# Kernel optimization log

Measured on AMD Instinct MI355X. Metric: run time of the kernel, lower is better.

Reference implementation:

```python
import jax, jax.numpy as jnp
import numpy as np

N_NODES = 100000
N_EDGES = 640000
D = 128
N_LAYERS = 4
N_GRAPHS = 512


def setup_inputs() -> dict:
    key = jax.random.key(0)
    ks = jax.random.split(key, 12)
    x = jax.random.normal(ks[0], (N_NODES, D), dtype=jnp.float32)
    edge_index = jax.random.randint(ks[1], (2, N_EDGES), 0, N_NODES, dtype=jnp.int64)
    batch = jnp.sort(jax.random.randint(ks[2], (N_NODES,), 0, N_GRAPHS, dtype=jnp.int64))
    s = 1.0 / np.sqrt(D)
    convW = jax.random.uniform(ks[3], (N_LAYERS, D, D), jnp.float32, -s, s)
    convB = jax.random.uniform(ks[4], (N_LAYERS, D), jnp.float32, -s, s)
    W1 = jax.random.uniform(ks[5], (D, D), jnp.float32, -s, s)
    b1 = jax.random.uniform(ks[6], (D,), jnp.float32, -s, s)
    W2 = jax.random.uniform(ks[7], (D, D), jnp.float32, -s, s)
    b2 = jax.random.uniform(ks[8], (D,), jnp.float32, -s, s)
    W3 = jax.random.uniform(ks[9], (D, 1), jnp.float32, -s, s)
    b3 = jax.random.uniform(ks[10], (1,), jnp.float32, -s, s)
    return {"x": x, "edge_index": edge_index, "batch": batch,
            "convW": convW, "convB": convB,
            "W1": W1, "b1": b1, "W2": W2, "b2": b2, "W3": W3, "b3": b3}


def reference(x, edge_index, batch, convW, convB, W1, b1, W2, b2, W3, b3):
    N = x.shape[0]
    # GCNConv default: add self-loops, symmetric deg^-1/2 normalization
    loops = jnp.arange(N, dtype=edge_index.dtype)
    src = jnp.concatenate([edge_index[0], loops])  # [E+N]
    dst = jnp.concatenate([edge_index[1], loops])
    deg = jax.ops.segment_sum(jnp.ones_like(dst, dtype=x.dtype), dst, num_segments=N)
    dinv = jnp.where(deg > 0, jax.lax.rsqrt(deg), 0.0)
    norm = (dinv[src] * dinv[dst])[:, None]  # [E+N, 1]
    h = x
    for i in range(N_LAYERS):
        hw = h @ convW[i]                                   # [N, D]
        msg = hw[src] * norm                                # gather + scale [E+N, D]
        agg = jax.ops.segment_sum(msg, dst, num_segments=N)  # scatter-add [N, D]
        h = jax.nn.relu(agg + convB[i])
    pooled = jax.ops.segment_sum(h, batch, num_segments=N_GRAPHS)  # [G, D]
    z = jax.nn.relu(pooled @ W1 + b1)
    z = jax.nn.relu(z @ W2 + b2)
    return jax.nn.sigmoid(z @ W3 + b3)  # [G, 1]
```

## Files before the change

kernel.cpp:

```cpp
#include <hip/hip_runtime.h>
#include <math.h>

#define D 128
#define LSTRIDE 136

typedef _Float16 half8 __attribute__((ext_vector_type(8)));
typedef _Float16 half4v __attribute__((ext_vector_type(4)));
typedef float f32x4 __attribute__((ext_vector_type(4)));


__global__ void k_fat1(const int* __restrict__ ei, int* __restrict__ counts,
                       int* __restrict__ pidx, int E, int countBlocks,
                       const float* __restrict__ convW, _Float16* __restrict__ Wf) {
    if ((int)blockIdx.x < countBlocks) {
        int e0 = (blockIdx.x * blockDim.x + threadIdx.x) * 4;
        if (e0 + 3 < E) {
            int4 d4 = *(const int4*)(ei + E + e0);
            int4 p;
            p.x = atomicAdd(&counts[d4.x], 1);
            p.y = atomicAdd(&counts[d4.y], 1);
            p.z = atomicAdd(&counts[d4.z], 1);
            p.w = atomicAdd(&counts[d4.w], 1);
            *(int4*)(pidx + e0) = p;
        } else {
            for (int e = e0; e < E; e++) pidx[e] = atomicAdd(&counts[ei[E + e]], 1);
        }
    } else {
        const int bid = blockIdx.x - countBlocks;
        const int l = bid >> 3;
        const int slot = (bid & 7) * 256 + threadIdx.x;
        const float* W = convW + (size_t)l * D * D;
        const int p = slot >> 6, ln = slot & 63;
        const int s = p >> 3, c = p & 7;
        const int kbase = s * 32 + ((ln >> 4) << 3);
        const int n = (c << 4) + (ln & 15);
        half8 hv;
#pragma unroll
        for (int j = 0; j < 8; j++) hv[j] = (_Float16)W[(size_t)(kbase + j) * D + n];
        *(half8*)(Wf + (size_t)l * D * D + (size_t)slot * 8) = hv;
    }
}

__global__ __launch_bounds__(256) void k_scan1(const int* __restrict__ counts,
                                               int* __restrict__ rowptrP,
                                               int* __restrict__ bsums,
                                               float* __restrict__ dinv,
                                               int* __restrict__ degHist, int N) {
    __shared__ int sh[256];
    __shared__ int lh[64];
    const int t = threadIdx.x;
    const int base = blockIdx.x * 1024 + t * 4;
    int c[4], pj[4];
#pragma unroll
    for (int j = 0; j < 4; j++) {
        c[j] = (base + j < N) ? counts[base + j] : 0;
        pj[j] = (c[j] + 3) & ~3;
    }
#pragma unroll
    for (int j = 0; j < 4; j++)
        if (base + j < N) dinv[base + j] = rsqrtf((float)(c[j] + 1));

    if (t < 64) lh[t] = 0;
    __syncthreads();
#pragma unroll
    for (int j = 0; j < 4; j++)
        if (base + j < N) atomicAdd(&lh[c[j] < 63 ? c[j] : 63], 1);
    __syncthreads();
    if (t < 64 && lh[t]) atomicAdd(&degHist[t], lh[t]);

    int tsum = pj[0] + pj[1] + pj[2] + pj[3];
    sh[t] = tsum;
    __syncthreads();
    for (int off = 1; off < 256; off <<= 1) {
        int v = (t >= off) ? sh[t - off] : 0;
        __syncthreads();
        sh[t] += v;
        __syncthreads();
    }
    int run = (t == 0) ? 0 : sh[t - 1];
    if (t == 255) bsums[blockIdx.x] = sh[255];
#pragma unroll
    for (int j = 0; j < 4; j++) {
        if (base + j <= N) rowptrP[base + j] = run;
        run += pj[j];
    }
}


__global__ __launch_bounds__(256) void k_fat2(int* __restrict__ rowptrP,
                                              const int* __restrict__ counts,
                                              const int* __restrict__ bsums,
                                              int NB, int N, int scanBlocks,
                                              const int* __restrict__ degHist,
                                              int* __restrict__ degCur,
                                              int* __restrict__ perm,
                                              int* __restrict__ rankOf) {
    if ((int)blockIdx.x < scanBlocks) {
        __shared__ int pre[128];
        const int t = threadIdx.x;
        if (t < 128) pre[t] = (t < NB) ? bsums[t] : 0;
        __syncthreads();
        for (int off = 1; off < 128; off <<= 1) {
            int v = (t >= off && t < 128) ? pre[t - off] : 0;
            __syncthreads();
            if (t < 128) pre[t] += v;
            __syncthreads();
        }
        int i = blockIdx.x * blockDim.x + t;
        if (i <= N) {
            int b = i >> 10;
            int add = (b == 0) ? 0 : pre[b - 1];
            rowptrP[i] += add;
        }
    } else {
        __shared__ int lbase[64], lh[64], gb[64];
        const int t = threadIdx.x;
        const int i = ((int)blockIdx.x - scanBlocks) * blockDim.x + t;
        if (t < 64) lh[t] = 0;
        __syncthreads();
        int deg = 0, lrank = 0;
        const bool v = i < N;
        if (v) {
            int c = counts[i];
            deg = c < 63 ? c : 63;
            lrank = atomicAdd(&lh[deg], 1);
        }
        __syncthreads();
        if (t < 64) gb[t] = lh[t] ? atomicAdd(&degCur[t], lh[t]) : 0;
        if (t == 0) {
            int run = 0;
            for (int d = 63; d >= 0; d--) { lbase[d] = run; run += degHist[d]; }
        }
        __syncthreads();
        if (v) {
            int r = 1 + lbase[deg] + gb[deg] + lrank;
            perm[r] = i;
            rankOf[i] = r;
        }
    }
}


__global__ void k_fill(const int* __restrict__ ei, const int* __restrict__ rowptrP,
                       const int* __restrict__ pidx, int* __restrict__ srcs, int E,
                       int fillBlocks, int N, int NS,
                       const int* __restrict__ rankOf,
                       const int* __restrict__ perm,
                       const float* __restrict__ dinv,
                       int* __restrict__ rbegR, int* __restrict__ rpenR,
                       float* __restrict__ dinvR, int* __restrict__ sentIdx,
                       const float* __restrict__ x,
                       _Float16* __restrict__ gA, _Float16* __restrict__ gB) {
    const int b = blockIdx.x;
    if (b < fillBlocks) {
        int e0 = (b * blockDim.x + threadIdx.x) * 4;
        if (e0 + 3 < E) {
            int4 s4 = *(const int4*)(ei + e0);
            int4 d4 = *(const int4*)(ei + E + e0);
            int4 p4 = *(const int4*)(pidx + e0);
            srcs[rowptrP[d4.x] + p4.x] = rankOf[s4.x];
            srcs[rowptrP[d4.y] + p4.y] = rankOf[s4.y];
            srcs[rowptrP[d4.z] + p4.z] = rankOf[s4.z];
            srcs[rowptrP[d4.w] + p4.w] = rankOf[s4.w];
        } else {
            for (int e = e0; e < E; e++)
                srcs[rowptrP[ei[E + e]] + pidx[e]] = rankOf[ei[e]];
        }
    } else {
        __shared__ int pS[16];
        __shared__ float dS[16];
        const int base = (b - fillBlocks) * 16;
        const int t = threadIdx.x;
        if (t == 0 && base == 0) {
            int4 sv; sv.x = sv.y = sv.z = sv.w = 0; *(int4*)sentIdx = sv;
        }
        if (t < 16) {
            const int r = base + t;
            int p = -1; float dv = 0.f;
            if (r >= 1 && r <= N) {
                p = perm[r];
                rbegR[r] = rowptrP[p];
                rpenR[r] = rowptrP[p + 1];
                dv = dinv[p];
                dinvR[r] = dv;
            } else if (r < NS) {
                rbegR[r] = 0; rpenR[r] = 0; dinvR[r] = 0.f;
            }
            pS[t] = p; dS[t] = dv;
        }
        __syncthreads();
        const int rr = base + (t >> 4);
        if (rr >= NS) return;
        const int j = t & 15;
        const int p = pS[t >> 4];
        if (p >= 0) {
            const float s = dS[t >> 4];
            const float4 v0 = *(const float4*)(x + (size_t)p * D + j * 8);
            const float4 v1 = *(const float4*)(x + (size_t)p * D + j * 8 + 4);
            half8 h;
            h[0] = (_Float16)(v0.x * s); h[1] = (_Float16)(v0.y * s);
            h[2] = (_Float16)(v0.z * s); h[3] = (_Float16)(v0.w * s);
            h[4] = (_Float16)(v1.x * s); h[5] = (_Float16)(v1.y * s);
            h[6] = (_Float16)(v1.z * s); h[7] = (_Float16)(v1.w * s);
            *(half8*)(gA + (size_t)rr * D + j * 8) = h;
        } else {
            half8 z;
#pragma unroll
            for (int j2 = 0; j2 < 8; j2++) z[j2] = (_Float16)0.f;
            *(half8*)(gA + (size_t)rr * D + j * 8) = z;
            *(half8*)(gB + (size_t)rr * D + j * 8) = z;
        }
    }
}


__global__ __launch_bounds__(256, 8) void k_layer(
        const _Float16* __restrict__ gin,
        const int* __restrict__ rbegR, const int* __restrict__ rpenR,
        const int* __restrict__ srcs,
        const int* __restrict__ sentIdx,
        const float* __restrict__ dinvR,
        const int* __restrict__ perm,
        const _Float16* __restrict__ Wf,
        const float* __restrict__ bias,
        _Float16* __restrict__ gout, int N, int last) {
    __shared__ _Float16 S[32 * LSTRIDE];

    const int tid  = threadIdx.x;
    const int w    = tid >> 6;
    const int lane = tid & 63;
    const int q    = lane >> 4;
    const int l16  = lane & 15;
    const int sb   = blockIdx.x * 32;
    const int cb   = l16 * 8;
    const int slot0 = sb + w * 8 + q * 2;

    int bg[2], nc[2];
    int mx = 0;
#pragma unroll
    for (int it = 0; it < 2; it++) {
        bg[it] = rbegR[slot0 + it];
        nc[it] = (rpenR[slot0 + it] - bg[it]) >> 2;
        mx = nc[it] > mx ? nc[it] : mx;
    }

    float a[2][8];
#pragma unroll
    for (int it = 0; it < 2; it++) {
        half8 sv = *(const half8*)(gin + (size_t)(slot0 + it) * D + cb);
#pragma unroll
        for (int j = 0; j < 8; j++) a[it][j] = (float)sv[j];
    }

    int4 cur[2];
#pragma unroll
    for (int it = 0; it < 2; it++) {
        const int* ip = (0 < nc[it]) ? (srcs + bg[it]) : sentIdx;
        cur[it] = *(const int4*)ip;
    }
    for (int ch = 0; ch < mx; ch++) {
        int4 nxt[2];
#pragma unroll
        for (int it = 0; it < 2; it++) {
            const int* ip = (ch + 1 < nc[it]) ? (srcs + bg[it] + (ch + 1) * 4) : sentIdx;
            nxt[it] = *(const int4*)ip;
        }
#pragma unroll
        for (int it = 0; it < 2; it++) {
            half8 v0 = *(const half8*)(gin + (size_t)cur[it].x * D + cb);
            half8 v1 = *(const half8*)(gin + (size_t)cur[it].y * D + cb);
            half8 v2 = *(const half8*)(gin + (size_t)cur[it].z * D + cb);
            half8 v3 = *(const half8*)(gin + (size_t)cur[it].w * D + cb);
#pragma unroll
            for (int j = 0; j < 8; j++)
                a[it][j] += ((float)v0[j] + (float)v1[j]) + ((float)v2[j] + (float)v3[j]);
        }
#pragma unroll
        for (int it = 0; it < 2; it++) cur[it] = nxt[it];
    }

#pragma unroll
    for (int it = 0; it < 2; it++) {
        const float sc = dinvR[slot0 + it];
        const int nl = w * 8 + q * 2 + it;
        half8 o;
#pragma unroll
        for (int j = 0; j < 8; j++) o[j] = (_Float16)(a[it][j] * sc);
        *(half8*)(&S[nl * LSTRIDE + cb]) = o;
    }

    __syncthreads();

    f32x4 acc[4];
#pragma unroll
    for (int c2 = 0; c2 < 4; c2++) acc[c2] = (f32x4){0.f, 0.f, 0.f, 0.f};

    const int tile = w >> 1;
    const int ccb  = (w & 1) * 4;
    const int nl2  = tile * 16 + l16;
#pragma unroll
    for (int s = 0; s < 4; s++) {
        half8 bf = *(const half8*)(&S[nl2 * LSTRIDE + s * 32 + q * 8]);
#pragma unroll
        for (int c2 = 0; c2 < 4; c2++) {
            half8 wh = *(const half8*)(Wf + (size_t)((s * 8 + ccb + c2) * 64 + lane) * 8);
            acc[c2] = __builtin_amdgcn_mfma_f32_16x16x32_f16(wh, bf, acc[c2], 0, 0, 0);
        }
    }

    const int slot2 = sb + nl2;
    if (!last) {
        const float scale = dinvR[slot2];
        _Float16* rp = gout + (size_t)slot2 * D + q * 4;
#pragma unroll
        for (int c2 = 0; c2 < 4; c2++) {
            const int cc = ccb + c2;
            const float4 bc = *(const float4*)(bias + cc * 16 + q * 4);
            half4v o;
            o[0] = (_Float16)(fmaxf(acc[c2][0] + bc.x, 0.f) * scale);
            o[1] = (_Float16)(fmaxf(acc[c2][1] + bc.y, 0.f) * scale);
            o[2] = (_Float16)(fmaxf(acc[c2][2] + bc.z, 0.f) * scale);
            o[3] = (_Float16)(fmaxf(acc[c2][3] + bc.w, 0.f) * scale);
            *(half4v*)(rp + cc * 16) = o;
        }
    } else if (slot2 >= 1 && slot2 <= N) {
        const int node2 = perm[slot2];
        _Float16* rp = gout + (size_t)node2 * D + q * 4;
#pragma unroll
        for (int c2 = 0; c2 < 4; c2++) {
            const int cc = ccb + c2;
            const float4 bc = *(const float4*)(bias + cc * 16 + q * 4);
            half4v o;
            o[0] = (_Float16)fmaxf(acc[c2][0] + bc.x, 0.f);
            o[1] = (_Float16)fmaxf(acc[c2][1] + bc.y, 0.f);
            o[2] = (_Float16)fmaxf(acc[c2][2] + bc.z, 0.f);
            o[3] = (_Float16)fmaxf(acc[c2][3] + bc.w, 0.f);
            *(half4v*)(rp + cc * 16) = o;
        }
    }
}


__global__ __launch_bounds__(256) void k_poolhead(
        const _Float16* __restrict__ h, const int* __restrict__ batch,
        const float* __restrict__ W1, const float* __restrict__ b1,
        const float* __restrict__ W2, const float* __restrict__ b2,
        const float* __restrict__ W3, const float* __restrict__ b3,
        float* __restrict__ out, int N) {
    __shared__ int sb[2];
    __shared__ float part[16][D];
    __shared__ float pool[D];
    __shared__ float z[D];
    __shared__ float red[D];
    __shared__ float pr[2][D];

    const int g = blockIdx.x;
    const int t = threadIdx.x;

    if (t < 2) {
        int target = g + t;
        int lo = 0, hi = N;
        while (lo < hi) {
            int mid = (lo + hi) >> 1;
            if (batch[mid] < target) lo = mid + 1; else hi = mid;
        }
        sb[t] = lo;
    }
    __syncthreads();
    const int rs = sb[0], re = sb[1];

    const int w = t >> 6;
    const int lane = t & 63;
    const int rw = w * 4 + (lane >> 4);
    const int c8 = (lane & 15) * 8;

    float ax[8];
#pragma unroll
    for (int j = 0; j < 8; j++) ax[j] = 0.f;
    for (int r = rs + rw; r < re; r += 16) {
        half8 vv = *(const half8*)(h + (size_t)r * D + c8);
#pragma unroll
        for (int j = 0; j < 8; j++) ax[j] += (float)vv[j];
    }
#pragma unroll
    for (int j = 0; j < 8; j++) part[rw][c8 + j] = ax[j];
    __syncthreads();

    if (t < D) {
        float s = 0.f;
#pragma unroll
        for (int gg = 0; gg < 16; gg++) s += part[gg][t];
        pool[t] = s;
    }
    __syncthreads();

    {
        const int hf = t >> 7, tt = t & 127;
        const int k0 = hf * 64;
        float s = 0.f;
        for (int k = k0; k < k0 + 64; k++) s = fmaf(pool[k], W1[(size_t)k * D + tt], s);
        pr[hf][tt] = s;
    }
    __syncthreads();
    if (t < D) z[t] = fmaxf(pr[0][t] + pr[1][t] + b1[t], 0.f);
    __syncthreads();

    {
        const int hf = t >> 7, tt = t & 127;
        const int k0 = hf * 64;
        float s = 0.f;
        for (int k = k0; k < k0 + 64; k++) s = fmaf(z[k], W2[(size_t)k * D + tt], s);
        pr[hf][tt] = s;
    }
    __syncthreads();
    if (t < D) red[t] = fmaxf(pr[0][t] + pr[1][t] + b2[t], 0.f) * W3[t];
    __syncthreads();
    for (int off = 64; off >= 1; off >>= 1) {
        if (t < off) red[t] += red[t + off];
        __syncthreads();
    }
    if (t == 0) out[g] = 1.f / (1.f + expf(-(red[0] + b3[0])));
}


extern "C" void kernel_launch(void* const* d_in, const int* in_sizes, int n_in,
                              void* d_out, int out_size, void* d_ws, size_t ws_size,
                              hipStream_t stream) {
    const float* x     = (const float*)d_in[0];
    const int*   ei    = (const int*)d_in[1];
    const int*   batch = (const int*)d_in[2];
    const float* convW = (const float*)d_in[3];
    const float* convB = (const float*)d_in[4];
    const float* W1 = (const float*)d_in[5];
    const float* b1 = (const float*)d_in[6];
    const float* W2 = (const float*)d_in[7];
    const float* b2 = (const float*)d_in[8];
    const float* W3 = (const float*)d_in[9];
    const float* b3 = (const float*)d_in[10];
    float* out = (float*)d_out;

    const int N = in_sizes[0] / D;
    const int E = in_sizes[1] / 2;
    const int G = out_size;
    const int NB = (N + 1023) / 1024;
    const int NS = ((N + 1 + 63) / 64) * 64;

    char* w = (char*)d_ws;
    size_t off = 0;
    auto alloc = [&](size_t bytes) -> char* {
        char* p = w + off;
        off += (bytes + 255) & ~(size_t)255;
        return p;
    };
    float*     dinv   = (float*)alloc((size_t)N * 4);
    _Float16*  gA     = (_Float16*)alloc((size_t)NS * D * 2);
    _Float16*  gB     = (_Float16*)alloc((size_t)NS * D * 2);
    _Float16*  Wf     = (_Float16*)alloc((size_t)4 * D * D * 2);
    int*       counts = (int*)alloc((size_t)(N + 128) * 4);
    int*       degHist= counts + N;
    int*       degCur = counts + N + 64;
    int*       rowptrP= (int*)alloc((size_t)(N + 1) * 4);
    int*       pidx   = (int*)alloc((size_t)E * 4);
    int*       srcs   = (int*)alloc((size_t)(E + 3 * N) * 4);
    int*       bsums  = (int*)alloc((size_t)NB * 4);
    int*       perm   = (int*)alloc((size_t)(N + 1) * 4);
    int*       rankOf = (int*)alloc((size_t)N * 4);
    int*       rbegR  = (int*)alloc((size_t)NS * 4);
    int*       rpenR  = (int*)alloc((size_t)NS * 4);
    float*     dinvR  = (float*)alloc((size_t)NS * 4);
    int*       sentIdx= (int*)alloc(16);

    hipMemsetAsync(counts, 0, (size_t)(N + 128) * 4, stream);
    hipMemsetAsync(srcs, 0, (size_t)(E + 3 * N) * 4, stream);
    const int countBlocks = (E / 4 + 255) / 256;
    k_fat1<<<countBlocks + 32, 256, 0, stream>>>(ei, counts, pidx, E, countBlocks,
                                                 convW, Wf);
    k_scan1<<<NB, 256, 0, stream>>>(counts, rowptrP, bsums, dinv, degHist, N);
    const int scanBlocks = (N + 1 + 255) / 256;
    const int rankBlocks = (N + 255) / 256;
    k_fat2<<<scanBlocks + rankBlocks, 256, 0, stream>>>(rowptrP, counts, bsums, NB, N,
                                                        scanBlocks,
                                                        degHist, degCur, perm, rankOf);
    const int fillBlocks = (E / 4 + 255) / 256;
    const int rowBlocks  = NS / 16;
    k_fill<<<fillBlocks + rowBlocks, 256, 0, stream>>>(
        ei, rowptrP, pidx, srcs, E, fillBlocks, N, NS,
        rankOf, perm, dinv, rbegR, rpenR, dinvR, sentIdx, x, gA, gB);

    const int layer_grid = NS / 32;
    const _Float16* gi = gA;
    _Float16* go = gB;
    for (int l = 0; l < 4; l++) {
        k_layer<<<layer_grid, 256, 0, stream>>>(gi, rbegR, rpenR, srcs, sentIdx,
                                                dinvR, perm,
                                                Wf + (size_t)l * D * D,
                                                convB + (size_t)l * D,
                                                go, N, l == 3);
        const _Float16* tmp = go;
        go = (_Float16*)gi;
        gi = tmp;
    }

    k_poolhead<<<G, 256, 0, stream>>>(gi, batch, W1, b1, W2, b2, W3, b3, out, N);
}
```

Measured before the change: 343.6 us.

## Build CSR via two-level bucket sort instead of global atomic counting

Edges are first histogrammed into 256-node destination buckets using shared-memory atomics, scanned, and scattered into a bucket-ordered edge array. Per-bucket kernels then count degrees and fill the CSR source list using shared-memory cursors. This replaces the per-edge global atomics and random scattered writes with localized LDS atomics and more coherent writes. The cost is three extra kernel launches and an extra pass over an 8-byte-per-edge staging buffer, and the ordering of sources within each row becomes nondeterministic.

Result: faster. 336.0 us, median of 2 (-2.2%).

```diff
diff --git a/kernel.cpp b/kernel.cpp
--- a/kernel.cpp
+++ b/kernel.cpp
@@ -9,24 +9,36 @@
 typedef float f32x4 __attribute__((ext_vector_type(4)));
 
 
-__global__ void k_fat1(const int* __restrict__ ei, int* __restrict__ counts,
-                       int* __restrict__ pidx, int E, int countBlocks,
-                       const float* __restrict__ convW, _Float16* __restrict__ Wf) {
-    if ((int)blockIdx.x < countBlocks) {
-        int e0 = (blockIdx.x * blockDim.x + threadIdx.x) * 4;
-        if (e0 + 3 < E) {
-            int4 d4 = *(const int4*)(ei + E + e0);
-            int4 p;
-            p.x = atomicAdd(&counts[d4.x], 1);
-            p.y = atomicAdd(&counts[d4.y], 1);
-            p.z = atomicAdd(&counts[d4.z], 1);
-            p.w = atomicAdd(&counts[d4.w], 1);
-            *(int4*)(pidx + e0) = p;
-        } else {
-            for (int e = e0; e < E; e++) pidx[e] = atomicAdd(&counts[ei[E + e]], 1);
-        }
+__global__ __launch_bounds__(256) void k_bhist(const int* __restrict__ ei, int E,
+                                               int edgeBlocks, int NBUK,
+                                               int* __restrict__ bukCnt,
+                                               const float* __restrict__ convW,
+                                               _Float16* __restrict__ Wf) {
+    if ((int)blockIdx.x < edgeBlocks) {
+        __shared__ int lh[512];
+        const int t = threadIdx.x;
+        for (int i = t; i < NBUK; i += 256) lh[i] = 0;
+        __syncthreads();
+        const int base = blockIdx.x * 4096;
+#pragma unroll
+        for (int k = 0; k < 4; k++) {
+            const int e0 = base + k * 1024 + t * 4;
+            if (e0 + 3 < E) {
+                int4 d4 = *(const int4*)(ei + E + e0);
+                atomicAdd(&lh[d4.x >> 8], 1);
+                atomicAdd(&lh[d4.y >> 8], 1);
+                atomicAdd(&lh[d4.z >> 8], 1);
+                atomicAdd(&lh[d4.w >> 8], 1);
+            } else {
+                for (int e = e0; e < E && e < e0 + 4; e++)
+                    atomicAdd(&lh[ei[E + e] >> 8], 1);
+            }
+        }
+        __syncthreads();
+        for (int i = t; i < NBUK; i += 256)
+            if (lh[i]) atomicAdd(&bukCnt[i], lh[i]);
     } else {
-        const int bid = blockIdx.x - countBlocks;
+        const int bid = blockIdx.x - edgeBlocks;
         const int l = bid >> 3;
         const int slot = (bid & 7) * 256 + threadIdx.x;
         const float* W = convW + (size_t)l * D * D;
@@ -39,6 +51,93 @@
         for (int j = 0; j < 8; j++) hv[j] = (_Float16)W[(size_t)(kbase + j) * D + n];
         *(half8*)(Wf + (size_t)l * D * D + (size_t)slot * 8) = hv;
     }
+}
+
+
+__global__ __launch_bounds__(512) void k_bscan(const int* __restrict__ bukCnt,
+                                               int* __restrict__ bukPtr,
+                                               int* __restrict__ bukCur, int NBUK) {
+    __shared__ int sh[512];
+    const int t = threadIdx.x;
+    sh[t] = (t < NBUK) ? bukCnt[t] : 0;
+    __syncthreads();
+    for (int off = 1; off < 512; off <<= 1) {
+        int v = (t >= off) ? sh[t - off] : 0;
+        __syncthreads();
+        sh[t] += v;
+        __syncthreads();
+    }
+    if (t < NBUK) {
+        int excl = (t == 0) ? 0 : sh[t - 1];
+        bukPtr[t] = excl;
+        bukCur[t] = excl;
+    }
+    if (t == NBUK) bukPtr[t] = sh[NBUK - 1];
+    else if (NBUK < 512 && t == 511 && NBUK == 512) {}
+}
+
+
+__global__ __launch_bounds__(256) void k_bscat(const int* __restrict__ ei, int E,
+                                               int NBUK, int* __restrict__ bukCur,
+                                               int2* __restrict__ ebuk) {
+    __shared__ int lcnt[512];
+    __shared__ int lbase[512];
+    const int t = threadIdx.x;
+    for (int i = t; i < NBUK; i += 256) lcnt[i] = 0;
+    __syncthreads();
+    const int base = blockIdx.x * 4096;
+    int es[16], ed[16], lr[16];
+#pragma unroll
+    for (int k = 0; k < 4; k++) {
+        const int e0 = base + k * 1024 + t * 4;
+        if (e0 + 3 < E) {
+            int4 s4 = *(const int4*)(ei + e0);
+            int4 d4 = *(const int4*)(ei + E + e0);
+            es[k * 4 + 0] = s4.x; ed[k * 4 + 0] = d4.x;
+            es[k * 4 + 1] = s4.y; ed[k * 4 + 1] = d4.y;
+            es[k * 4 + 2] = s4.z; ed[k * 4 + 2] = d4.z;
+            es[k * 4 + 3] = s4.w; ed[k * 4 + 3] = d4.w;
+        } else {
+#pragma unroll
+            for (int j = 0; j < 4; j++) {
+                const int e = e0 + j;
+                if (e < E) { es[k * 4 + j] = ei[e]; ed[k * 4 + j] = ei[E + e]; }
+                else ed[k * 4 + j] = -1;
+            }
+        }
+    }
+#pragma unroll
+    for (int i = 0; i < 16; i++)
+        if (ed[i] >= 0) lr[i] = atomicAdd(&lcnt[ed[i] >> 8], 1);
+    __syncthreads();
+    for (int i = t; i < NBUK; i += 256)
+        lbase[i] = lcnt[i] ? atomicAdd(&bukCur[i], lcnt[i]) : 0;
+    __syncthreads();
+#pragma unroll
+    for (int i = 0; i < 16; i++) {
+        if (ed[i] >= 0) {
+            int2 e2; e2.x = es[i]; e2.y = ed[i];
+            ebuk[lbase[ed[i] >> 8] + lr[i]] = e2;
+        }
+    }
+}
+
+
+__global__ __launch_bounds__(256) void k_bcount(const int2* __restrict__ ebuk,
+                                                const int* __restrict__ bukPtr,
+                                                int* __restrict__ counts, int N) {
+    __shared__ int cnt[256];
+    const int b = blockIdx.x, t = threadIdx.x;
+    cnt[t] = 0;
+    __syncthreads();
+    const int beg = bukPtr[b], end = bukPtr[b + 1];
+    for (int i = beg + t; i < end; i += 256) {
+        int2 e = ebuk[i];
+        atomicAdd(&cnt[e.y & 255], 1);
+    }
+    __syncthreads();
+    const int node = b * 256 + t;
+    if (node < N) counts[node] = cnt[t];
 }
 
 __global__ __launch_bounds__(256) void k_scan1(const int* __restrict__ counts,
@@ -141,35 +240,32 @@
 }
 
 
-__global__ void k_fill(const int* __restrict__ ei, const int* __restrict__ rowptrP,
-                       const int* __restrict__ pidx, int* __restrict__ srcs, int E,
-                       int fillBlocks, int N, int NS,
-                       const int* __restrict__ rankOf,
-                       const int* __restrict__ perm,
-                       const float* __restrict__ dinv,
-                       int* __restrict__ rbegR, int* __restrict__ rpenR,
-                       float* __restrict__ dinvR, int* __restrict__ sentIdx,
-                       const float* __restrict__ x,
-                       _Float16* __restrict__ gA, _Float16* __restrict__ gB) {
+__global__ void k_bfill(const int2* __restrict__ ebuk, const int* __restrict__ bukPtr,
+                        const int* __restrict__ rowptrP, int* __restrict__ srcs,
+                        const int* __restrict__ rankOf, int NBUK, int N, int NS,
+                        const int* __restrict__ perm,
+                        const float* __restrict__ dinv,
+                        int* __restrict__ rbegR, int* __restrict__ rpenR,
+                        float* __restrict__ dinvR, int* __restrict__ sentIdx,
+                        const float* __restrict__ x,
+                        _Float16* __restrict__ gA, _Float16* __restrict__ gB) {
     const int b = blockIdx.x;
-    if (b < fillBlocks) {
-        int e0 = (b * blockDim.x + threadIdx.x) * 4;
-        if (e0 + 3 < E) {
-            int4 s4 = *(const int4*)(ei + e0);
-            int4 d4 = *(const int4*)(ei + E + e0);
-            int4 p4 = *(const int4*)(pidx + e0);
-            srcs[rowptrP[d4.x] + p4.x] = rankOf[s4.x];
-            srcs[rowptrP[d4.y] + p4.y] = rankOf[s4.y];
-            srcs[rowptrP[d4.z] + p4.z] = rankOf[s4.z];
-            srcs[rowptrP[d4.w] + p4.w] = rankOf[s4.w];
-        } else {
-            for (int e = e0; e < E; e++)
-                srcs[rowptrP[ei[E + e]] + pidx[e]] = rankOf[ei[e]];
+    if (b < NBUK) {
+        __shared__ int cur[256];
+        const int t = threadIdx.x;
+        const int node = b * 256 + t;
+        cur[t] = (node < N) ? rowptrP[node] : 0;
+        __syncthreads();
+        const int beg = bukPtr[b], end = bukPtr[b + 1];
+        for (int i = beg + t; i < end; i += 256) {
+            int2 e = ebuk[i];
+            int p = atomicAdd(&cur[e.y & 255], 1);
+            srcs[p] = rankOf[e.x];
         }
     } else {
         __shared__ int pS[16];
         __shared__ float dS[16];
-        const int base = (b - fillBlocks) * 16;
+        const int base = (b - NBUK) * 16;
         const int t = threadIdx.x;
         if (t == 0 && base == 0) {
             int4 sv; sv.x = sv.y = sv.z = sv.w = 0; *(int4*)sentIdx = sv;
@@ -444,6 +540,7 @@
     const int G = out_size;
     const int NB = (N + 1023) / 1024;
     const int NS = ((N + 1 + 63) / 64) * 64;
+    const int NBUK = (N + 255) / 256;
 
     char* w = (char*)d_ws;
     size_t off = 0;
@@ -456,11 +553,15 @@
     _Float16*  gA     = (_Float16*)alloc((size_t)NS * D * 2);
     _Float16*  gB     = (_Float16*)alloc((size_t)NS * D * 2);
     _Float16*  Wf     = (_Float16*)alloc((size_t)4 * D * D * 2);
-    int*       counts = (int*)alloc((size_t)(N + 128) * 4);
-    int*       degHist= counts + N;
-    int*       degCur = counts + N + 64;
+    int*       counts = (int*)alloc((size_t)N * 4);
+    int*       misc   = (int*)alloc((size_t)(512 + 64 + 64) * 4);
+    int*       bukCnt = misc;
+    int*       degHist= misc + 512;
+    int*       degCur = misc + 576;
+    int*       bukPtr = (int*)alloc((size_t)(NBUK + 1) * 4);
+    int*       bukCur = (int*)alloc((size_t)NBUK * 4);
+    int2*      ebuk   = (int2*)alloc((size_t)E * 8);
     int*       rowptrP= (int*)alloc((size_t)(N + 1) * 4);
-    int*       pidx   = (int*)alloc((size_t)E * 4);
     int*       srcs   = (int*)alloc((size_t)(E + 3 * N) * 4);
     int*       bsums  = (int*)alloc((size_t)NB * 4);
     int*       perm   = (int*)alloc((size_t)(N + 1) * 4);
@@ -470,22 +571,24 @@
     float*     dinvR  = (float*)alloc((size_t)NS * 4);
     int*       sentIdx= (int*)alloc(16);
 
-    hipMemsetAsync(counts, 0, (size_t)(N + 128) * 4, stream);
+    hipMemsetAsync(misc, 0, (size_t)(512 + 64 + 64) * 4, stream);
     hipMemsetAsync(srcs, 0, (size_t)(E + 3 * N) * 4, stream);
-    const int countBlocks = (E / 4 + 255) / 256;
-    k_fat1<<<countBlocks + 32, 256, 0, stream>>>(ei, counts, pidx, E, countBlocks,
+    const int edgeBlocks = (E + 4095) / 4096;
+    k_bhist<<<edgeBlocks + 32, 256, 0, stream>>>(ei, E, edgeBlocks, NBUK, bukCnt,
                                                  convW, Wf);
+    k_bscan<<<1, 512, 0, stream>>>(bukCnt, bukPtr, bukCur, NBUK);
+    k_bscat<<<edgeBlocks, 256, 0, stream>>>(ei, E, NBUK, bukCur, ebuk);
+    k_bcount<<<NBUK, 256, 0, stream>>>(ebuk, bukPtr, counts, N);
     k_scan1<<<NB, 256, 0, stream>>>(counts, rowptrP, bsums, dinv, degHist, N);
     const int scanBlocks = (N + 1 + 255) / 256;
     const int rankBlocks = (N + 255) / 256;
     k_fat2<<<scanBlocks + rankBlocks, 256, 0, stream>>>(rowptrP, counts, bsums, NB, N,
                                                         scanBlocks,
                                                         degHist, degCur, perm, rankOf);
-    const int fillBlocks = (E / 4 + 255) / 256;
-    const int rowBlocks  = NS / 16;
-    k_fill<<<fillBlocks + rowBlocks, 256, 0, stream>>>(
-        ei, rowptrP, pidx, srcs, E, fillBlocks, N, NS,
-        rankOf, perm, dinv, rbegR, rpenR, dinvR, sentIdx, x, gA, gB);
+    const int rowBlocks = NS / 16;
+    k_bfill<<<NBUK + rowBlocks, 256, 0, stream>>>(
+        ebuk, bukPtr, rowptrP, srcs, rankOf, NBUK, N, NS,
+        perm, dinv, rbegR, rpenR, dinvR, sentIdx, x, gA, gB);
 
     const int layer_grid = NS / 32;
     const _Float16* gi = gA;
```
